# Optimization experiments

Hardware: AMD Instinct MI355X
Metric: run time of the kernel (lower is better)

## Reference

```python
import jax, jax.numpy as jnp
import numpy as np

TOPK = 8
N_GROUPS = 8
TOPK_GROUPS = 4
ROUTE_SCALE = 2.5


def setup_inputs() -> dict:
    key = jax.random.key(0)
    k1, k2, k3 = jax.random.split(key, 3)
    T, D, E = 8192, 7168, 256
    x = jax.random.normal(k1, (T, D), dtype=jnp.float32)
    weight = jax.random.normal(k2, (E, D), dtype=jnp.float32) * 0.02
    bias = jax.random.normal(k3, (E,), dtype=jnp.float32) * 0.01
    return {"x": x, "weight": weight, "bias": bias}


def reference(x, weight, bias):
    T = x.shape[0]
    E = weight.shape[0]
    # gate GEMM in fp32 (x.float() @ weight.float().T) + sigmoid scoring
    scores = jax.nn.sigmoid(jnp.einsum('td,ed->te', x, weight))  # [T, E]
    original_scores = scores
    s = scores + bias  # bias only affects routing decisions, not weights
    # group-limited routing: [T, n_groups, experts_per_group]
    sg = s.reshape(T, N_GROUPS, E // N_GROUPS)
    # bias branch: group score = sum of top-2 expert scores within group
    group_scores = jax.lax.top_k(sg, 2)[0].sum(axis=-1)  # [T, G]
    gidx = jax.lax.top_k(group_scores, TOPK_GROUPS)[1]   # [T, topk_groups]
    keep = jnp.zeros((T, N_GROUPS), dtype=bool).at[
        jnp.arange(T)[:, None], gidx].set(True)
    masked = jnp.where(keep[:, :, None], sg, -jnp.inf).reshape(T, E)
    indices = jax.lax.top_k(masked, TOPK)[1]  # [T, topk]
    weights = jnp.take_along_axis(original_scores, indices, axis=1)
    weights = weights / weights.sum(axis=-1, keepdims=True)  # sigmoid norm
    weights = weights * ROUTE_SCALE
    return weights, indices
```

## Files before the change

### kernel.cpp

```cpp
#include <hip/hip_runtime.h>
#include <math.h>

#define T_TOK 8192
#define D_DIM 7168
#define E_EXP 256
#define TOPKN 8
#define NGRP 8
#define GSIZE 32
#define TOPG 4
#define ROUTE_SCALEF 2.5f

#define KSPLIT 4
#define KPER (D_DIM / KSPLIT)
#define BM 128
#define BK 32
#define NTILE (KPER / BK)

typedef _Float16 f16;
typedef f16 f16x8 __attribute__((ext_vector_type(8)));
typedef f16 f16x4 __attribute__((ext_vector_type(4)));
typedef float f32x4 __attribute__((ext_vector_type(4)));

__global__ __launch_bounds__(256)
void split_w(const float* __restrict__ W, f16* __restrict__ Wh, f16* __restrict__ Wl) {
  int i = blockIdx.x * 256 + threadIdx.x;
  float4 v = ((const float4*)W)[i];
  float pe[4] = {v.x, v.y, v.z, v.w};
  f16x4 h, l;
#pragma unroll
  for (int m = 0; m < 4; ++m) {
    f16 hh = (f16)pe[m];
    float rc = pe[m] - (float)hh;
    h[m] = hh;
    l[m] = (f16)(rc * 4096.0f);
  }
  ((f16x4*)Wh)[i] = h;
  ((f16x4*)Wl)[i] = l;
}

__device__ __forceinline__ void gload_lds16(const void* g, void* l) {
  __builtin_amdgcn_global_load_lds(
      (const __attribute__((address_space(1))) unsigned int*)g,
      (__attribute__((address_space(3))) unsigned int*)l, 16, 0, 0);
}

__global__ __launch_bounds__(512, 2)
void gate_gemm(const float* __restrict__ X, const f16* __restrict__ Wh,
               const f16* __restrict__ Wl, float* __restrict__ partial) {
  __shared__ f16 Ah[BM][BK], Al[BM][BK];
  __shared__ f16 Bh[E_EXP][BK], Bl[E_EXP][BK];

  const int tid  = threadIdx.x;
  const int lane = tid & 63;
  const int wid  = tid >> 6;
  const int mb   = blockIdx.x;
  const int ks   = blockIdx.y;
  const int kbase = ks * KPER;

  const int ar = tid >> 2;
  const int ak = (tid & 3) * 8;
  const float* Xp = X + (size_t)(mb * BM + ar) * D_DIM + kbase + ak;

  const int bc0 = wid * 2;
  const int be  = lane >> 2;
  const int bk  = (lane & 3) * 8;
  const f16* Whp = Wh + (size_t)(bc0 * 16 + be) * D_DIM + kbase + bk;
  const f16* Wlp = Wl + (size_t)(bc0 * 16 + be) * D_DIM + kbase + bk;

  const int wm0 = (wid >> 2) * 64;
  const int wn0 = (wid & 3) * 64;
  const int fr  = lane & 15;
  const int fk  = (lane >> 4) * 8;

  f32x4 accA[4][4], accB[4][4];
#pragma unroll
  for (int i = 0; i < 4; ++i)
#pragma unroll
    for (int j = 0; j < 4; ++j) {
      accA[i][j] = f32x4{0.f, 0.f, 0.f, 0.f};
      accB[i][j] = f32x4{0.f, 0.f, 0.f, 0.f};
    }

  float4 pa0 = *(const float4*)(Xp);
  float4 pa1 = *(const float4*)(Xp + 4);

#pragma unroll 1
  for (int kt = 0; kt < NTILE; ++kt) {
    const int kc = kt * BK;

    gload_lds16(Whp + kc,                        &Bh[bc0 * 16][0]);
    gload_lds16(Whp + kc + (size_t)16 * D_DIM,   &Bh[(bc0 + 1) * 16][0]);
    gload_lds16(Wlp + kc,                        &Bl[bc0 * 16][0]);
    gload_lds16(Wlp + kc + (size_t)16 * D_DIM,   &Bl[(bc0 + 1) * 16][0]);

    float pe[8] = {pa0.x, pa0.y, pa0.z, pa0.w, pa1.x, pa1.y, pa1.z, pa1.w};
    f16x8 hv, lv;
#pragma unroll
    for (int m = 0; m < 8; ++m) {
      f16 h = (f16)pe[m];
      float rc = pe[m] - (float)h;
      hv[m] = h;
      lv[m] = (f16)(rc * 4096.0f);
    }
    *(f16x8*)&Ah[ar][ak] = hv;
    *(f16x8*)&Al[ar][ak] = lv;

    if (kt + 1 < NTILE) {
      pa0 = *(const float4*)(Xp + kc + BK);
      pa1 = *(const float4*)(Xp + kc + BK + 4);
    }

    __syncthreads();

    f16x8 b_h[4], b_l[4], a_h[4], a_l[4];
#pragma unroll
    for (int j = 0; j < 4; ++j) {
      b_h[j] = *(const f16x8*)&Bh[wn0 + j * 16 + fr][fk];
      b_l[j] = *(const f16x8*)&Bl[wn0 + j * 16 + fr][fk];
    }
#pragma unroll
    for (int i = 0; i < 4; ++i) {
      a_h[i] = *(const f16x8*)&Ah[wm0 + i * 16 + fr][fk];
      a_l[i] = *(const f16x8*)&Al[wm0 + i * 16 + fr][fk];
    }
#pragma unroll
    for (int i = 0; i < 4; ++i)
#pragma unroll
      for (int j = 0; j < 4; ++j) {
        accA[i][j] = __builtin_amdgcn_mfma_f32_16x16x32_f16(a_h[i], b_h[j], accA[i][j], 0, 0, 0);
        accB[i][j] = __builtin_amdgcn_mfma_f32_16x16x32_f16(a_h[i], b_l[j], accB[i][j], 0, 0, 0);
        accB[i][j] = __builtin_amdgcn_mfma_f32_16x16x32_f16(a_l[i], b_h[j], accB[i][j], 0, 0, 0);
      }

    __syncthreads();
  }

  const float s = 1.0f / 4096.0f;
  float* pout = partial + (size_t)ks * T_TOK * E_EXP;
#pragma unroll
  for (int i = 0; i < 4; ++i) {
    const int row0 = mb * BM + wm0 + i * 16 + (lane >> 4) * 4;
#pragma unroll
    for (int j = 0; j < 4; ++j) {
      const int col = wn0 + j * 16 + fr;
      f32x4 v = accA[i][j] + accB[i][j] * s;
#pragma unroll
      for (int r = 0; r < 4; ++r)
        pout[(size_t)(row0 + r) * E_EXP + col] = v[r];
    }
  }
}

__global__ __launch_bounds__(256)
void reduce_sigmoid(const float* __restrict__ partial, float* __restrict__ scores) {
  const int g = blockIdx.x * 256 + threadIdx.x;
  const int Q = T_TOK * E_EXP / 4;
  const float4* p = (const float4*)partial;
  float4 a = p[g], b = p[g + Q], c = p[g + 2 * Q], d = p[g + 3 * Q];
  float4 o;
  o.x = 1.f / (1.f + expf(-(a.x + b.x + c.x + d.x)));
  o.y = 1.f / (1.f + expf(-(a.y + b.y + c.y + d.y)));
  o.z = 1.f / (1.f + expf(-(a.z + b.z + c.z + d.z)));
  o.w = 1.f / (1.f + expf(-(a.w + b.w + c.w + d.w)));
  ((float4*)scores)[g] = o;
}

__global__ __launch_bounds__(256)
void gate_route(const float* __restrict__ scores, const float* __restrict__ bias,
                float* __restrict__ wout, float* __restrict__ iout, int T) {
  int t = blockIdx.x * blockDim.x + threadIdx.x;
  if (t >= T) return;
  const float* srow = scores + (size_t)t * E_EXP;

  float gs[NGRP];
#pragma unroll
  for (int g = 0; g < NGRP; ++g) {
    float m1 = -INFINITY, m2 = -INFINITY;
#pragma unroll 1
    for (int e = 0; e < GSIZE; ++e) {
      float v = srow[g * GSIZE + e] + bias[g * GSIZE + e];
      if (v > m1) { m2 = m1; m1 = v; }
      else if (v > m2) { m2 = v; }
    }
    gs[g] = m1 + m2;
  }

  int keepmask = 0;
#pragma unroll
  for (int r = 0; r < TOPG; ++r) {
    float bv = -INFINITY; int best = 0;
#pragma unroll
    for (int g = 0; g < NGRP; ++g) {
      bool used = (keepmask >> g) & 1;
      if (!used && gs[g] > bv) { bv = gs[g]; best = g; }
    }
    keepmask |= (1 << best);
  }

  float val[TOPKN]; int idx[TOPKN];
#pragma unroll
  for (int i = 0; i < TOPKN; ++i) { val[i] = -INFINITY; idx[i] = -1; }
#pragma unroll 1
  for (int g = 0; g < NGRP; ++g) {
    bool kept = (keepmask >> g) & 1;
#pragma unroll 1
    for (int e = 0; e < GSIZE; ++e) {
      int ex = g * GSIZE + e;
      float v = kept ? (srow[ex] + bias[ex]) : -INFINITY;
      if (v > val[TOPKN - 1]) {
        val[TOPKN - 1] = v; idx[TOPKN - 1] = ex;
#pragma unroll
        for (int p = TOPKN - 1; p > 0; --p) {
          if (val[p] > val[p - 1]) {
            float tv = val[p]; val[p] = val[p - 1]; val[p - 1] = tv;
            int   ti = idx[p]; idx[p] = idx[p - 1]; idx[p - 1] = ti;
          }
        }
      }
    }
  }

  float w[TOPKN]; float sum = 0.f;
#pragma unroll
  for (int i = 0; i < TOPKN; ++i) { w[i] = srow[idx[i]]; sum += w[i]; }
#pragma unroll
  for (int i = 0; i < TOPKN; ++i) {
    wout[(size_t)t * TOPKN + i] = (w[i] / sum) * ROUTE_SCALEF;
    iout[(size_t)t * TOPKN + i] = (float)idx[i];
  }
}

extern "C" void kernel_launch(void* const* d_in, const int* in_sizes, int n_in,
                              void* d_out, int out_size, void* d_ws, size_t ws_size,
                              hipStream_t stream) {
  const float* x  = (const float*)d_in[0];
  const float* w  = (const float*)d_in[1];
  const float* b  = (const float*)d_in[2];
  float* out      = (float*)d_out;

  f16*   Wh      = (f16*)d_ws;
  f16*   Wl      = Wh + (size_t)E_EXP * D_DIM;
  float* partial = (float*)(Wl + (size_t)E_EXP * D_DIM);
  float* scores  = partial + (size_t)KSPLIT * T_TOK * E_EXP;

  split_w<<<E_EXP * D_DIM / 4 / 256, 256, 0, stream>>>(w, Wh, Wl);

  dim3 gg(T_TOK / BM, KSPLIT);
  gate_gemm<<<gg, 512, 0, stream>>>(x, Wh, Wl, partial);

  reduce_sigmoid<<<T_TOK * E_EXP / 4 / 256, 256, 0, stream>>>(partial, scores);

  float* wout = out;
  float* iout = out + (size_t)T_TOK * TOPKN;
  gate_route<<<(T_TOK + 255) / 256, 256, 0, stream>>>(scores, b, wout, iout, T_TOK);
}
```

Before: 488.9 us.

## Swizzle LDS, merge accumulators, raise k-split, fuse reduce+sigmoid into wave-per-token routing

The weight split kernel now pre-swizzles the f16 hi/lo columns so that LDS reads of both A and B avoid bank conflicts. It also rescales the hi/lo parts by 64 so all three MFMA products can share one accumulator, which halves accumulator registers and allows occupancy of 4 waves per SIMD. When the workspace is large enough, the split-K factor is raised to 8. The separate reduce_sigmoid pass is folded into a new wave-per-token routing kernel that does the reductions with shuffles. The risks are changed fp16 rounding behaviour from the scaling and more partial-sum traffic with the larger k-split.

```diff
diff --git a/kernel.cpp b/kernel.cpp
--- a/kernel.cpp
+++ b/kernel.cpp
@@ -6,36 +6,37 @@
 #define E_EXP 256
 #define TOPKN 8
 #define NGRP 8
-#define GSIZE 32
 #define TOPG 4
 #define ROUTE_SCALEF 2.5f
 
-#define KSPLIT 4
-#define KPER (D_DIM / KSPLIT)
 #define BM 128
 #define BK 32
-#define NTILE (KPER / BK)
 
 typedef _Float16 f16;
 typedef f16 f16x8 __attribute__((ext_vector_type(8)));
-typedef f16 f16x4 __attribute__((ext_vector_type(4)));
 typedef float f32x4 __attribute__((ext_vector_type(4)));
 
 __global__ __launch_bounds__(256)
 void split_w(const float* __restrict__ W, f16* __restrict__ Wh, f16* __restrict__ Wl) {
-  int i = blockIdx.x * 256 + threadIdx.x;
-  float4 v = ((const float4*)W)[i];
-  float pe[4] = {v.x, v.y, v.z, v.w};
-  f16x4 h, l;
-#pragma unroll
-  for (int m = 0; m < 4; ++m) {
-    f16 hh = (f16)pe[m];
-    float rc = pe[m] - (float)hh;
-    h[m] = hh;
-    l[m] = (f16)(rc * 4096.0f);
-  }
-  ((f16x4*)Wh)[i] = h;
-  ((f16x4*)Wl)[i] = l;
+  const int e  = blockIdx.x;
+  const int se = (e >> 1) & 3;
+  for (int s = threadIdx.x; s < D_DIM / 8; s += 256) {
+    const int t = s >> 2, c = s & 3;
+    const int kin  = t * 32 + ((c ^ se) << 3);
+    const int kout = t * 32 + (c << 3);
+    const float4 v0 = *(const float4*)(W + (size_t)e * D_DIM + kin);
+    const float4 v1 = *(const float4*)(W + (size_t)e * D_DIM + kin + 4);
+    const float pe[8] = {v0.x, v0.y, v0.z, v0.w, v1.x, v1.y, v1.z, v1.w};
+    f16x8 h, l;
+#pragma unroll
+    for (int m = 0; m < 8; ++m) {
+      const float hf = (float)(f16)pe[m];
+      h[m] = (f16)(hf * 64.0f);
+      l[m] = (f16)((pe[m] - hf) * 64.0f);
+    }
+    *(f16x8*)(Wh + (size_t)e * D_DIM + kout) = h;
+    *(f16x8*)(Wl + (size_t)e * D_DIM + kout) = l;
+  }
 }
 
 __device__ __forceinline__ void gload_lds16(const void* g, void* l) {
@@ -44,94 +45,94 @@
       (__attribute__((address_space(3))) unsigned int*)l, 16, 0, 0);
 }
 
-__global__ __launch_bounds__(512, 2)
+__global__ __launch_bounds__(512, 4)
 void gate_gemm(const float* __restrict__ X, const f16* __restrict__ Wh,
-               const f16* __restrict__ Wl, float* __restrict__ partial) {
+               const f16* __restrict__ Wl, float* __restrict__ partial, int kper) {
   __shared__ f16 Ah[BM][BK], Al[BM][BK];
   __shared__ f16 Bh[E_EXP][BK], Bl[E_EXP][BK];
 
-  const int tid  = threadIdx.x;
-  const int lane = tid & 63;
-  const int wid  = tid >> 6;
-  const int mb   = blockIdx.x;
-  const int ks   = blockIdx.y;
-  const int kbase = ks * KPER;
-
-  const int ar = tid >> 2;
-  const int ak = (tid & 3) * 8;
-  const float* Xp = X + (size_t)(mb * BM + ar) * D_DIM + kbase + ak;
-
-  const int bc0 = wid * 2;
-  const int be  = lane >> 2;
-  const int bk  = (lane & 3) * 8;
-  const f16* Whp = Wh + (size_t)(bc0 * 16 + be) * D_DIM + kbase + bk;
-  const f16* Wlp = Wl + (size_t)(bc0 * 16 + be) * D_DIM + kbase + bk;
+  const int tid   = threadIdx.x;
+  const int lane  = tid & 63;
+  const int wid   = tid >> 6;
+  const int mb    = blockIdx.x;
+  const int ks    = blockIdx.y;
+  const int kbase = ks * kper;
+  const int ntile = kper >> 5;
+
+  const int sr = wid * 16 + (lane & 15);
+  const int sc = lane >> 4;
+  const float* Xp = X + (size_t)(mb * BM + sr) * D_DIM + kbase + (sc << 3);
+  const int awoff = ((sc ^ ((sr >> 1) & 3)) << 3);
+
+  const f16* Whp = Wh + (size_t)(wid * 32 + (lane >> 2)) * D_DIM + kbase + ((lane & 3) << 3);
+  const f16* Wlp = Wl + (size_t)(wid * 32 + (lane >> 2)) * D_DIM + kbase + ((lane & 3) << 3);
 
   const int wm0 = (wid >> 2) * 64;
   const int wn0 = (wid & 3) * 64;
   const int fr  = lane & 15;
-  const int fk  = (lane >> 4) * 8;
-
-  f32x4 accA[4][4], accB[4][4];
+  const int rdoff = (((lane >> 4) << 3)) ^ (((fr >> 1) & 3) << 3);
+
+  f32x4 acc[4][4];
 #pragma unroll
   for (int i = 0; i < 4; ++i)
 #pragma unroll
-    for (int j = 0; j < 4; ++j) {
-      accA[i][j] = f32x4{0.f, 0.f, 0.f, 0.f};
-      accB[i][j] = f32x4{0.f, 0.f, 0.f, 0.f};
-    }
+    for (int j = 0; j < 4; ++j) acc[i][j] = f32x4{0.f, 0.f, 0.f, 0.f};
 
   float4 pa0 = *(const float4*)(Xp);
   float4 pa1 = *(const float4*)(Xp + 4);
 
 #pragma unroll 1
-  for (int kt = 0; kt < NTILE; ++kt) {
-    const int kc = kt * BK;
-
-    gload_lds16(Whp + kc,                        &Bh[bc0 * 16][0]);
-    gload_lds16(Whp + kc + (size_t)16 * D_DIM,   &Bh[(bc0 + 1) * 16][0]);
-    gload_lds16(Wlp + kc,                        &Bl[bc0 * 16][0]);
-    gload_lds16(Wlp + kc + (size_t)16 * D_DIM,   &Bl[(bc0 + 1) * 16][0]);
-
-    float pe[8] = {pa0.x, pa0.y, pa0.z, pa0.w, pa1.x, pa1.y, pa1.z, pa1.w};
+  for (int kt = 0; kt < ntile; ++kt) {
+    const int kc = kt << 5;
+
+    gload_lds16(Whp + kc,                      &Bh[wid * 32][0]);
+    gload_lds16(Whp + kc + (size_t)16 * D_DIM, &Bh[wid * 32 + 16][0]);
+    gload_lds16(Wlp + kc,                      &Bl[wid * 32][0]);
+    gload_lds16(Wlp + kc + (size_t)16 * D_DIM, &Bl[wid * 32 + 16][0]);
+
+    const int knext = (kt + 1 < ntile) ? kc + 32 : kc;
+    const float4 na0 = *(const float4*)(Xp + knext);
+    const float4 na1 = *(const float4*)(Xp + knext + 4);
+
+    const float pe[8] = {pa0.x, pa0.y, pa0.z, pa0.w, pa1.x, pa1.y, pa1.z, pa1.w};
     f16x8 hv, lv;
 #pragma unroll
     for (int m = 0; m < 8; ++m) {
-      f16 h = (f16)pe[m];
-      float rc = pe[m] - (float)h;
-      hv[m] = h;
-      lv[m] = (f16)(rc * 4096.0f);
-    }
-    *(f16x8*)&Ah[ar][ak] = hv;
-    *(f16x8*)&Al[ar][ak] = lv;
-
-    if (kt + 1 < NTILE) {
-      pa0 = *(const float4*)(Xp + kc + BK);
-      pa1 = *(const float4*)(Xp + kc + BK + 4);
-    }
+      const float hf = (float)(f16)pe[m];
+      hv[m] = (f16)(hf * 64.0f);
+      lv[m] = (f16)((pe[m] - hf) * 64.0f);
+    }
+    *(f16x8*)&Ah[sr][awoff] = hv;
+    *(f16x8*)&Al[sr][awoff] = lv;
+    pa0 = na0; pa1 = na1;
 
     __syncthreads();
 
-    f16x8 b_h[4], b_l[4], a_h[4], a_l[4];
-#pragma unroll
-    for (int j = 0; j < 4; ++j) {
-      b_h[j] = *(const f16x8*)&Bh[wn0 + j * 16 + fr][fk];
-      b_l[j] = *(const f16x8*)&Bl[wn0 + j * 16 + fr][fk];
-    }
+    f16x8 bh0 = *(const f16x8*)&Bh[wn0 +  0 + fr][rdoff];
+    f16x8 bl0 = *(const f16x8*)&Bl[wn0 +  0 + fr][rdoff];
+    f16x8 bh1 = *(const f16x8*)&Bh[wn0 + 16 + fr][rdoff];
+    f16x8 bl1 = *(const f16x8*)&Bl[wn0 + 16 + fr][rdoff];
+    f16x8 bh2 = *(const f16x8*)&Bh[wn0 + 32 + fr][rdoff];
+    f16x8 bl2 = *(const f16x8*)&Bl[wn0 + 32 + fr][rdoff];
+    f16x8 bh3 = *(const f16x8*)&Bh[wn0 + 48 + fr][rdoff];
+    f16x8 bl3 = *(const f16x8*)&Bl[wn0 + 48 + fr][rdoff];
 #pragma unroll
     for (int i = 0; i < 4; ++i) {
-      a_h[i] = *(const f16x8*)&Ah[wm0 + i * 16 + fr][fk];
-      a_l[i] = *(const f16x8*)&Al[wm0 + i * 16 + fr][fk];
-    }
-#pragma unroll
-    for (int i = 0; i < 4; ++i)
-#pragma unroll
-      for (int j = 0; j < 4; ++j) {
-        accA[i][j] = __builtin_amdgcn_mfma_f32_16x16x32_f16(a_h[i], b_h[j], accA[i][j], 0, 0, 0);
-        accB[i][j] = __builtin_amdgcn_mfma_f32_16x16x32_f16(a_h[i], b_l[j], accB[i][j], 0, 0, 0);
-        accB[i][j] = __builtin_amdgcn_mfma_f32_16x16x32_f16(a_l[i], b_h[j], accB[i][j], 0, 0, 0);
-      }
-
+      const f16x8 ah = *(const f16x8*)&Ah[wm0 + i * 16 + fr][rdoff];
+      const f16x8 al = *(const f16x8*)&Al[wm0 + i * 16 + fr][rdoff];
+      acc[i][0] = __builtin_amdgcn_mfma_f32_16x16x32_f16(ah, bh0, acc[i][0], 0, 0, 0);
+      acc[i][0] = __builtin_amdgcn_mfma_f32_16x16x32_f16(ah, bl0, acc[i][0], 0, 0, 0);
+      acc[i][0] = __builtin_amdgcn_mfma_f32_16x16x32_f16(al, bh0, acc[i][0], 0, 0, 0);
+      acc[i][1] = __builtin_amdgcn_mfma_f32_16x16x32_f16(ah, bh1, acc[i][1], 0, 0, 0);
+      acc[i][1] = __builtin_amdgcn_mfma_f32_16x16x32_f16(ah, bl1, acc[i][1], 0, 0, 0);
+      acc[i][1] = __builtin_amdgcn_mfma_f32_16x16x32_f16(al, bh1, acc[i][1], 0, 0, 0);
+      acc[i][2] = __builtin_amdgcn_mfma_f32_16x16x32_f16(ah, bh2, acc[i][2], 0, 0, 0);
+      acc[i][2] = __builtin_amdgcn_mfma_f32_16x16x32_f16(ah, bl2, acc[i][2], 0, 0, 0);
+      acc[i][2] = __builtin_amdgcn_mfma_f32_16x16x32_f16(al, bh2, acc[i][2], 0, 0, 0);
+      acc[i][3] = __builtin_amdgcn_mfma_f32_16x16x32_f16(ah, bh3, acc[i][3], 0, 0, 0);
+      acc[i][3] = __builtin_amdgcn_mfma_f32_16x16x32_f16(ah, bl3, acc[i][3], 0, 0, 0);
+      acc[i][3] = __builtin_amdgcn_mfma_f32_16x16x32_f16(al, bh3, acc[i][3], 0, 0, 0);
+    }
     __syncthreads();
   }
 
@@ -143,7 +144,7 @@
 #pragma unroll
     for (int j = 0; j < 4; ++j) {
       const int col = wn0 + j * 16 + fr;
-      f32x4 v = accA[i][j] + accB[i][j] * s;
+      const f32x4 v = acc[i][j] * s;
 #pragma unroll
       for (int r = 0; r < 4; ++r)
         pout[(size_t)(row0 + r) * E_EXP + col] = v[r];
@@ -152,105 +153,110 @@
 }
 
 __global__ __launch_bounds__(256)
-void reduce_sigmoid(const float* __restrict__ partial, float* __restrict__ scores) {
-  const int g = blockIdx.x * 256 + threadIdx.x;
-  const int Q = T_TOK * E_EXP / 4;
-  const float4* p = (const float4*)partial;
-  float4 a = p[g], b = p[g + Q], c = p[g + 2 * Q], d = p[g + 3 * Q];
-  float4 o;
-  o.x = 1.f / (1.f + expf(-(a.x + b.x + c.x + d.x)));
-  o.y = 1.f / (1.f + expf(-(a.y + b.y + c.y + d.y)));
-  o.z = 1.f / (1.f + expf(-(a.z + b.z + c.z + d.z)));
-  o.w = 1.f / (1.f + expf(-(a.w + b.w + c.w + d.w)));
-  ((float4*)scores)[g] = o;
-}
-
-__global__ __launch_bounds__(256)
-void gate_route(const float* __restrict__ scores, const float* __restrict__ bias,
-                float* __restrict__ wout, float* __restrict__ iout, int T) {
-  int t = blockIdx.x * blockDim.x + threadIdx.x;
-  if (t >= T) return;
-  const float* srow = scores + (size_t)t * E_EXP;
-
-  float gs[NGRP];
-#pragma unroll
-  for (int g = 0; g < NGRP; ++g) {
-    float m1 = -INFINITY, m2 = -INFINITY;
-#pragma unroll 1
-    for (int e = 0; e < GSIZE; ++e) {
-      float v = srow[g * GSIZE + e] + bias[g * GSIZE + e];
-      if (v > m1) { m2 = m1; m1 = v; }
-      else if (v > m2) { m2 = v; }
-    }
-    gs[g] = m1 + m2;
-  }
-
+void gate_route(const float* __restrict__ partial, const float* __restrict__ bias,
+                float* __restrict__ wout, float* __restrict__ iout, int ksplit) {
+  const int t    = (blockIdx.x * 256 + threadIdx.x) >> 6;
+  const int lane = threadIdx.x & 63;
+
+  float sx = 0.f, sy = 0.f, sz = 0.f, sw = 0.f;
+  for (int ks = 0; ks < ksplit; ++ks) {
+    const float4 p = *(const float4*)(partial + ((size_t)ks * T_TOK + t) * E_EXP + (lane << 2));
+    sx += p.x; sy += p.y; sz += p.z; sw += p.w;
+  }
+  const float o0 = 1.f / (1.f + expf(-sx));
+  const float o1 = 1.f / (1.f + expf(-sy));
+  const float o2 = 1.f / (1.f + expf(-sz));
+  const float o3 = 1.f / (1.f + expf(-sw));
+  const float4 bv4 = *(const float4*)(bias + (lane << 2));
+  const float b0 = o0 + bv4.x, b1 = o1 + bv4.y, b2 = o2 + bv4.z, b3 = o3 + bv4.w;
+
+  const float ma = fmaxf(b0, b1), mi = fminf(b0, b1);
+  const float mb_ = fmaxf(b2, b3), mn = fminf(b2, b3);
+  float m1 = fmaxf(ma, mb_);
+  float m2 = fmaxf(fminf(ma, mb_), fmaxf(mi, mn));
+#pragma unroll
+  for (int msk = 1; msk <= 4; msk <<= 1) {
+    const float p1 = __shfl_xor(m1, msk);
+    const float p2 = __shfl_xor(m2, msk);
+    const float nm1 = fmaxf(m1, p1);
+    const float nm2 = fmaxf(fminf(m1, p1), fmaxf(m2, p2));
+    m1 = nm1; m2 = nm2;
+  }
+  const float gs = m1 + m2;
+
+  float ga[8];
+#pragma unroll
+  for (int g = 0; g < 8; ++g) ga[g] = __shfl(gs, g * 8);
   int keepmask = 0;
 #pragma unroll
   for (int r = 0; r < TOPG; ++r) {
-    float bv = -INFINITY; int best = 0;
+    float bvv = -INFINITY; int bg = 0;
 #pragma unroll
     for (int g = 0; g < NGRP; ++g) {
-      bool used = (keepmask >> g) & 1;
-      if (!used && gs[g] > bv) { bv = gs[g]; best = g; }
-    }
-    keepmask |= (1 << best);
-  }
-
-  float val[TOPKN]; int idx[TOPKN];
-#pragma unroll
-  for (int i = 0; i < TOPKN; ++i) { val[i] = -INFINITY; idx[i] = -1; }
-#pragma unroll 1
-  for (int g = 0; g < NGRP; ++g) {
-    bool kept = (keepmask >> g) & 1;
-#pragma unroll 1
-    for (int e = 0; e < GSIZE; ++e) {
-      int ex = g * GSIZE + e;
-      float v = kept ? (srow[ex] + bias[ex]) : -INFINITY;
-      if (v > val[TOPKN - 1]) {
-        val[TOPKN - 1] = v; idx[TOPKN - 1] = ex;
-#pragma unroll
-        for (int p = TOPKN - 1; p > 0; --p) {
-          if (val[p] > val[p - 1]) {
-            float tv = val[p]; val[p] = val[p - 1]; val[p - 1] = tv;
-            int   ti = idx[p]; idx[p] = idx[p - 1]; idx[p - 1] = ti;
-          }
-        }
-      }
-    }
-  }
-
-  float w[TOPKN]; float sum = 0.f;
-#pragma unroll
-  for (int i = 0; i < TOPKN; ++i) { w[i] = srow[idx[i]]; sum += w[i]; }
-#pragma unroll
-  for (int i = 0; i < TOPKN; ++i) {
-    wout[(size_t)t * TOPKN + i] = (w[i] / sum) * ROUTE_SCALEF;
-    iout[(size_t)t * TOPKN + i] = (float)idx[i];
+      const bool better = !((keepmask >> g) & 1) && (ga[g] > bvv);
+      bvv = better ? ga[g] : bvv;
+      bg  = better ? g : bg;
+    }
+    keepmask |= 1 << bg;
+  }
+
+  const bool kept = (keepmask >> (lane >> 3)) & 1;
+  const float c0 = kept ? b0 : -INFINITY;
+  const float c1 = kept ? b1 : -INFINITY;
+  const float c2 = kept ? b2 : -INFINITY;
+  const float c3 = kept ? b3 : -INFINITY;
+
+  int used = 0;
+  float sum = 0.f, selw = 0.f;
+  int seli = 0;
+#pragma unroll
+  for (int r = 0; r < TOPKN; ++r) {
+    float bv_ = -INFINITY; int bi_ = 0x7FFFFFFF; float bo_ = 0.f;
+    { const bool ok = !(used & 1) && (c0 > bv_); bv_ = ok ? c0 : bv_; bi_ = ok ? (lane << 2)     : bi_; bo_ = ok ? o0 : bo_; }
+    { const bool ok = !(used & 2) && (c1 > bv_); bv_ = ok ? c1 : bv_; bi_ = ok ? (lane << 2) | 1 : bi_; bo_ = ok ? o1 : bo_; }
+    { const bool ok = !(used & 4) && (c2 > bv_); bv_ = ok ? c2 : bv_; bi_ = ok ? (lane << 2) | 2 : bi_; bo_ = ok ? o2 : bo_; }
+    { const bool ok = !(used & 8) && (c3 > bv_); bv_ = ok ? c3 : bv_; bi_ = ok ? (lane << 2) | 3 : bi_; bo_ = ok ? o3 : bo_; }
+#pragma unroll
+    for (int m = 1; m < 64; m <<= 1) {
+      const float vp = __shfl_xor(bv_, m);
+      const int   ip = __shfl_xor(bi_, m);
+      const float op = __shfl_xor(bo_, m);
+      const bool take = (vp > bv_) || (vp == bv_ && ip < bi_);
+      bv_ = take ? vp : bv_; bi_ = take ? ip : bi_; bo_ = take ? op : bo_;
+    }
+    sum += bo_;
+    if (lane == r) { selw = bo_; seli = bi_; }
+    if ((bi_ >> 2) == lane) used |= 1 << (bi_ & 3);
+  }
+
+  if (lane < TOPKN) {
+    wout[(size_t)t * TOPKN + lane] = (selw / sum) * ROUTE_SCALEF;
+    iout[(size_t)t * TOPKN + lane] = (float)seli;
   }
 }
 
 extern "C" void kernel_launch(void* const* d_in, const int* in_sizes, int n_in,
                               void* d_out, int out_size, void* d_ws, size_t ws_size,
                               hipStream_t stream) {
-  const float* x  = (const float*)d_in[0];
-  const float* w  = (const float*)d_in[1];
-  const float* b  = (const float*)d_in[2];
-  float* out      = (float*)d_out;
-
-  f16*   Wh      = (f16*)d_ws;
-  f16*   Wl      = Wh + (size_t)E_EXP * D_DIM;
+  const float* x = (const float*)d_in[0];
+  const float* w = (const float*)d_in[1];
+  const float* b = (const float*)d_in[2];
+  float* out = (float*)d_out;
+
+  const size_t whl = (size_t)E_EXP * D_DIM * sizeof(f16);
+  const size_t per_split = (size_t)T_TOK * E_EXP * sizeof(float);
+  const int ksplit = (ws_size >= 2 * whl + 8 * per_split) ? 8 : 4;
+
+  f16* Wh = (f16*)d_ws;
+  f16* Wl = Wh + (size_t)E_EXP * D_DIM;
   float* partial = (float*)(Wl + (size_t)E_EXP * D_DIM);
-  float* scores  = partial + (size_t)KSPLIT * T_TOK * E_EXP;
-
-  split_w<<<E_EXP * D_DIM / 4 / 256, 256, 0, stream>>>(w, Wh, Wl);
-
-  dim3 gg(T_TOK / BM, KSPLIT);
-  gate_gemm<<<gg, 512, 0, stream>>>(x, Wh, Wl, partial);
-
-  reduce_sigmoid<<<T_TOK * E_EXP / 4 / 256, 256, 0, stream>>>(partial, scores);
+
+  split_w<<<E_EXP, 256, 0, stream>>>(w, Wh, Wl);
+
+  dim3 gg(T_TOK / BM, ksplit);
+  gate_gemm<<<gg, 512, 0, stream>>>(x, Wh, Wl, partial, D_DIM / ksplit);
 
   float* wout = out;
   float* iout = out + (size_t)T_TOK * TOPKN;
-  gate_route<<<(T_TOK + 255) / 256, 256, 0, stream>>>(scores, b, wout, iout, T_TOK);
-}
+  gate_route<<<T_TOK / 4, 256, 0, stream>>>(partial, b, wout, iout, ksplit);
+}
```

Result: faster. 412.4 us (-15.6%).
